# Kernel optimization log

Measured on AMD Instinct MI355X. Metric: run time of the kernel, lower is better.

Reference implementation:

```python
import jax, jax.numpy as jnp
import numpy as np

N_NODES = 100000
N_EDGES = 3200000
N_FEAT = 128
N_CLASS = 40
K_HOPS = 2


def setup_inputs() -> dict:
    key = jax.random.key(0)
    k1, k2, k3 = jax.random.split(key, 3)
    feature = jax.random.normal(k1, (N_NODES, N_FEAT), dtype=jnp.float32)
    # Glorot-ish linear params (SGConv.lin)
    weight = jax.random.normal(k2, (N_CLASS, N_FEAT), dtype=jnp.float32) * (1.0 / np.sqrt(N_FEAT))
    bias = jnp.zeros((N_CLASS,), dtype=jnp.float32)
    edge_index = jax.random.randint(k3, (2, N_EDGES), 0, N_NODES, dtype=jnp.int64)
    return {"feature": feature, "weight": weight, "bias": bias,
            "edge_index": edge_index, "use_feature": 1}


def reference(feature, weight, bias, edge_index, use_feature):
    # use_feature is a Python int flag; SGC uses feature when true (identity otherwise)
    x = feature if use_feature else jnp.eye(feature.shape[0], feature.shape[1], dtype=feature.dtype)
    N = x.shape[0]

    # gcn_norm: add self-loops, symmetric normalization D^-1/2 (A+I) D^-1/2
    loops = jnp.arange(N, dtype=edge_index.dtype)
    row = jnp.concatenate([edge_index[0], loops])  # source nodes
    col = jnp.concatenate([edge_index[1], loops])  # target nodes
    ew = jnp.ones(row.shape[0], dtype=x.dtype)
    deg = jax.ops.segment_sum(ew, col, num_segments=N)  # in-degree incl. self-loop
    deg_inv_sqrt = jnp.where(deg > 0, jax.lax.rsqrt(jnp.maximum(deg, 1e-12)), 0.0)
    norm = deg_inv_sqrt[row] * deg_inv_sqrt[col]  # [E+N]

    # K-hop propagation: out[col] += norm * x[row]
    for _ in range(K_HOPS):
        x = jax.ops.segment_sum(norm[:, None] * x[row], col, num_segments=N)

    logits = x @ weight.T + bias  # [N, C]
    return jax.nn.log_softmax(logits, axis=1)
```

## Files before the change

kernel.cpp:

```cpp
#include <hip/hip_runtime.h>
#include <hip/hip_bf16.h>
#include <hip/hip_fp16.h>
#include <math.h>


#define N_NODES 100000
#define N_FEAT  128
#define N_CLASS 40

#define RANGE   256
#define NBALLOC 512
#define NBUSED  391
#define RANGE_C 2048
#define NCALLOC 64
#define NCUSED  49
#define CAP     8704
#define CCAP    67072
#define P3AGRID 1024

typedef __attribute__((ext_vector_type(8))) short short8;
typedef __attribute__((ext_vector_type(4))) float floatx4;

__global__ void detect_zero_kernel(const int* __restrict__ ei, int* __restrict__ flag,
                                   int* __restrict__ bucketCount,
                                   int* __restrict__ coarseCnt) {
    int t = threadIdx.x;
    if (t < NBALLOC) bucketCount[t] = 0;
    if (t < NCALLOC) coarseCnt[t] = 0;
    if (t < 64) {
        int nz = (ei[2 * t + 1] != 0) ? 1 : 0;
        unsigned long long b = __ballot(nz);
        if (t == 0) *flag = (b == 0ull) ? 1 : 0;
    }
}

__device__ __forceinline__ int edge_word(const int* ei, int elem, int is64) {
    return is64 ? ei[2 * elem] : ei[elem];
}

__global__ __launch_bounds__(256) void p3a_scatter(
    const int* __restrict__ ei, int E, const int* __restrict__ flag,
    int* __restrict__ bucketCount, int* __restrict__ coarseCnt,
    unsigned int* __restrict__ tmpc)
{
    __shared__ int hf[NBALLOC];
    __shared__ int hc[NCALLOC];
    __shared__ int basec[NCALLOC];
    __shared__ int curc[NCALLOC];
    int t = threadIdx.x;
    for (int i = t; i < NBALLOC; i += 256) hf[i] = 0;
    if (t < NCALLOC) hc[t] = 0;
    __syncthreads();
    int is64 = *flag;
    int per = (E + gridDim.x - 1) / gridDim.x;
    int e0 = blockIdx.x * per;
    int e1 = min(E, e0 + per);
    for (int e = e0 + t; e < e1; e += 256) {
        int c = edge_word(ei, E + e, is64);
        atomicAdd(&hf[c >> 8], 1);
        atomicAdd(&hc[c >> 11], 1);
    }
    __syncthreads();
    if (t < NCALLOC) {
        basec[t] = hc[t] ? atomicAdd(&coarseCnt[t], hc[t]) : 0;
        curc[t] = 0;
    }
    for (int i = t; i < NBALLOC; i += 256)
        if (hf[i]) atomicAdd(&bucketCount[i], hf[i]);
    __syncthreads();
    for (int e = e0 + t; e < e1; e += 256) {
        int c = edge_word(ei, E + e, is64);
        int r = edge_word(ei, e, is64);
        int cb = c >> 11;
        int p = basec[cb] + atomicAdd(&curc[cb], 1);
        if (p < CCAP)
            tmpc[(size_t)cb * CCAP + p] = ((unsigned)(c & 2047) << 17) | (unsigned)r;
    }
}

__global__ __launch_bounds__(NBALLOC) void p2_scan(
    const int* __restrict__ bucketCount, int* __restrict__ bucketStart,
    int* __restrict__ bucketCursor, int* __restrict__ starts, int E)
{
    __shared__ int s[NBALLOC];
    int t = threadIdx.x;
    int v = bucketCount[t];
    s[t] = v;
    __syncthreads();
    for (int o = 1; o < NBALLOC; o <<= 1) {
        int y = (t >= o) ? s[t - o] : 0;
        __syncthreads();
        s[t] += y;
        __syncthreads();
    }
    int incl = s[t], excl = incl - v;
    bucketStart[t] = excl;
    bucketCursor[t] = excl;
    if (t == NBALLOC - 1) { bucketStart[NBALLOC] = incl; starts[N_NODES] = E; }
}

__global__ __launch_bounds__(256) void p3b_scatter(
    const unsigned int* __restrict__ tmpc, const int* __restrict__ coarseCnt,
    int* __restrict__ bucketCursor, unsigned int* __restrict__ tmp)
{
    __shared__ int fh[8];
    __shared__ int fb[8];
    __shared__ int fc[8];
    int cb = blockIdx.x >> 3;
    int j = blockIdx.x & 7;
    int t = threadIdx.x;
    int cnt = coarseCnt[cb];
    if (cnt > CCAP) cnt = CCAP;
    int chunk = (cnt + 7) >> 3;
    int r0 = j * chunk;
    int r1 = min(cnt, r0 + chunk);
    if (t < 8) fh[t] = 0;
    __syncthreads();
    const unsigned int* rec = tmpc + (size_t)cb * CCAP;
    for (int i = r0 + t; i < r1; i += 256) {
        int dlc = (int)(rec[i] >> 17);
        atomicAdd(&fh[dlc >> 8], 1);
    }
    __syncthreads();
    if (t < 8) {
        fb[t] = fh[t] ? atomicAdd(&bucketCursor[cb * 8 + t], fh[t]) : 0;
        fc[t] = 0;
    }
    __syncthreads();
    for (int i = r0 + t; i < r1; i += 256) {
        unsigned v = rec[i];
        int dlc = (int)(v >> 17);
        unsigned src = v & 0x1FFFFu;
        int fi = dlc >> 8;
        int dlf = dlc & 255;
        int p = fb[fi] + atomicAdd(&fc[fi], 1);
        tmp[p] = ((unsigned)dlf << 24) | src;
    }
}

__global__ __launch_bounds__(256) void p4_sort(
    const unsigned int* __restrict__ tmp, const int* __restrict__ bucketStart,
    int* __restrict__ starts, float* __restrict__ dis, int* __restrict__ srcsB, int N)
{
    __shared__ int srt[CAP];
    __shared__ int hist[256];
    __shared__ int sc[256];
    __shared__ int cur[256];
    int b = blockIdx.x, t = threadIdx.x;
    int g0 = b * RANGE;
    int gcnt = N - g0;
    if (gcnt > RANGE) gcnt = RANGE;
    int base = bucketStart[b];
    int n = bucketStart[b + 1] - base;
    hist[t] = 0;
    __syncthreads();
    for (int i = t; i < n; i += 256)
        atomicAdd(&hist[tmp[base + i] >> 24], 1);
    __syncthreads();
    int hv = hist[t];
    sc[t] = hv;
    __syncthreads();
    for (int o = 1; o < 256; o <<= 1) {
        int y = (t >= o) ? sc[t - o] : 0;
        __syncthreads();
        sc[t] += y;
        __syncthreads();
    }
    int excl = sc[t] - hv;
    if (t < gcnt) {
        starts[g0 + t] = base + excl;
        dis[g0 + t] = rsqrtf((float)(hv + 1));
    }
    cur[t] = excl;
    __syncthreads();
    if (n <= CAP) {
        for (int i = t; i < n; i += 256) {
            unsigned v = tmp[base + i];
            int p = atomicAdd(&cur[v >> 24], 1);
            srt[p] = (int)(v & 0xFFFFFFu) * 80;
        }
        __syncthreads();
        for (int i = t; i < n; i += 256) srcsB[base + i] = srt[i];
    } else {
        for (int i = t; i < n; i += 256) {
            unsigned v = tmp[base + i];
            int p = atomicAdd(&cur[v >> 24], 1);
            srcsB[base + p] = (int)(v & 0xFFFFFFu) * 80;
        }
    }
}

__device__ __forceinline__ unsigned short f2bf(float f) {
    unsigned u = __float_as_uint(f);
    unsigned r = u + 0x7FFFu + ((u >> 16) & 1u);
    return (unsigned short)(r >> 16);
}
__device__ __forceinline__ __half2 u2h(unsigned w) {
    union { unsigned u; __half2 h; } c; c.u = w; return c.h;
}
__device__ __forceinline__ unsigned h2u(__half2 h) {
    union { unsigned u; __half2 h; } c; c.h = h; return c.u;
}

__global__ __launch_bounds__(256) void transform_mfma(
    const float* __restrict__ x, const float* __restrict__ W,
    const float* __restrict__ dis, unsigned short* __restrict__ t0, int N)
{
    __shared__ uint4 Wl[3 * 4 * 64];
    int t = threadIdx.x;
    for (int i = t; i < 3 * 4 * 64; i += 256) {
        int lane = i & 63;
        int kc = (i >> 6) & 3;
        int nt = i >> 8;
        int n = nt * 16 + (lane & 15);
        int k = kc * 32 + (lane >> 4) * 8;
        union { unsigned short s[8]; uint4 v; } u;
        #pragma unroll
        for (int j = 0; j < 8; ++j)
            u.s[j] = (n < N_CLASS) ? f2bf(W[n * N_FEAT + k + j]) : (unsigned short)0;
        Wl[i] = u.v;
    }
    __syncthreads();
    int wave = (blockIdx.x * blockDim.x + threadIdx.x) >> 6;
    int lane = threadIdx.x & 63;
    int ntile = (N + 15) / 16;
    if (wave >= ntile) return;
    int m = lane & 15, quad = lane >> 4;
    int row = wave * 16 + m;
    const short8* Wf = reinterpret_cast<const short8*>(Wl);
    floatx4 acc0 = {0.f, 0.f, 0.f, 0.f}, acc1 = acc0, acc2 = acc0;
    #pragma unroll
    for (int kc = 0; kc < 4; ++kc) {
        const float4* xr = reinterpret_cast<const float4*>(
            x + (size_t)row * N_FEAT + kc * 32 + quad * 8);
        float4 a0 = xr[0], a1 = xr[1];
        short8 af;
        af[0] = f2bf(a0.x); af[1] = f2bf(a0.y); af[2] = f2bf(a0.z); af[3] = f2bf(a0.w);
        af[4] = f2bf(a1.x); af[5] = f2bf(a1.y); af[6] = f2bf(a1.z); af[7] = f2bf(a1.w);
        short8 b0 = Wf[(0 * 4 + kc) * 64 + lane];
        short8 b1 = Wf[(1 * 4 + kc) * 64 + lane];
        short8 b2 = Wf[(2 * 4 + kc) * 64 + lane];
        acc0 = __builtin_amdgcn_mfma_f32_16x16x32_bf16(af, b0, acc0, 0, 0, 0);
        acc1 = __builtin_amdgcn_mfma_f32_16x16x32_bf16(af, b1, acc1, 0, 0, 0);
        acc2 = __builtin_amdgcn_mfma_f32_16x16x32_bf16(af, b2, acc2, 0, 0, 0);
    }
    #pragma unroll
    for (int r = 0; r < 4; ++r) {
        int rw = wave * 16 + quad * 4 + r;
        float ds = dis[rw];
        unsigned short* tr = t0 + (size_t)rw * N_CLASS;
        tr[m] = __half_as_ushort(__float2half(ds * acc0[r]));
        tr[16 + m] = __half_as_ushort(__float2half(ds * acc1[r]));
        if (m < 8) tr[32 + m] = __half_as_ushort(__float2half(ds * acc2[r]));
    }
}

__device__ __forceinline__ __half2 foldh(__half2 a, int lane) {
    a = __hadd2(a, u2h((unsigned)__shfl((int)h2u(a), lane + 30)));
    a = __hadd2(a, u2h((unsigned)__shfl((int)h2u(a), lane + 15)));
    __half2 u = u2h((unsigned)__shfl((int)h2u(a), lane + 5));
    __half2 v = u2h((unsigned)__shfl((int)h2u(a), lane + 10));
    return __hadd2(__hadd2(a, u), v);
}

#define GATHER12H(tin)                                                         \
    int d = wave;                                                              \
    int g = lane / 5;                           \
    int sl = lane - g * 5;                                           \
    int slo = sl << 4;                             \
    int e0 = starts[d], e1 = starts[d + 1];                                    \
    const char* tb = (const char*)(tin);                                       \
    __half2 z2 = u2h(0u);                                                      \
    __half2 A0 = z2, A1 = z2, A2 = z2, A3 = z2;                                \
    __half2 B0 = z2, B1 = z2, B2 = z2, B3 = z2;                                \
    if (lane < 5) {                                       \
        uint4 r = *reinterpret_cast<const uint4*>(tb + d * 80 + slo);          \
        A0 = u2h(r.x); A1 = u2h(r.y); A2 = u2h(r.z); A3 = u2h(r.w);            \
    }                                                                          \
    int gg = (g < 12) ? g : 0;                      \
    int e = e0;                                                                \
    for (; e + 24 <= e1; e += 24) {         \
        int o1 = srcsB[e + gg];                                                \
        int o2 = srcsB[e + 12 + gg];                                           \
        uint4 r1 = *reinterpret_cast<const uint4*>(tb + (size_t)(unsigned)o1 + slo); \
        uint4 r2 = *reinterpret_cast<const uint4*>(tb + (size_t)(unsigned)o2 + slo); \
        A0 = __hadd2(A0, u2h(r1.x)); A1 = __hadd2(A1, u2h(r1.y));              \
        A2 = __hadd2(A2, u2h(r1.z)); A3 = __hadd2(A3, u2h(r1.w));              \
        B0 = __hadd2(B0, u2h(r2.x)); B1 = __hadd2(B1, u2h(r2.y));              \
        B2 = __hadd2(B2, u2h(r2.z)); B3 = __hadd2(B3, u2h(r2.w));              \
    }                                                                          \
    for (; e < e1; e += 12) {                      \
        int ee = e + gg;                                                       \
        int o1 = srcsB[min(ee, e1 - 1)];                                       \
        uint4 r1 = *reinterpret_cast<const uint4*>(tb + (size_t)(unsigned)o1 + slo); \
        if (!(ee < e1 && g < 12)) { r1.x = 0u; r1.y = 0u; r1.z = 0u; r1.w = 0u; } \
        A0 = __hadd2(A0, u2h(r1.x)); A1 = __hadd2(A1, u2h(r1.y));              \
        A2 = __hadd2(A2, u2h(r1.z)); A3 = __hadd2(A3, u2h(r1.w));              \
    }                                                                          \
    A0 = __hadd2(A0, B0); A1 = __hadd2(A1, B1);                                \
    A2 = __hadd2(A2, B2); A3 = __hadd2(A3, B3);                                \
    A0 = foldh(A0, lane); A1 = foldh(A1, lane);                                \
    A2 = foldh(A2, lane); A3 = foldh(A3, lane);

__global__ __launch_bounds__(256) void prop_hop_kernel(
    const unsigned short* __restrict__ tin, unsigned short* __restrict__ tout,
    const int* __restrict__ starts, const int* __restrict__ srcsB,
    const float* __restrict__ dis, int N)
{
    int wave = (blockIdx.x * blockDim.x + threadIdx.x) >> 6;
    int lane = threadIdx.x & 63;
    if (wave >= N) return;
    GATHER12H(tin)
    if (lane < 5) {
        float dd = dis[d];
        float sc = dd * dd;
        float2 f0 = __half22float2(A0), f1 = __half22float2(A1);
        float2 f2 = __half22float2(A2), f3 = __half22float2(A3);
        uint4 o;
        o.x = h2u(__floats2half2_rn(sc * f0.x, sc * f0.y));
        o.y = h2u(__floats2half2_rn(sc * f1.x, sc * f1.y));
        o.z = h2u(__floats2half2_rn(sc * f2.x, sc * f2.y));
        o.w = h2u(__floats2half2_rn(sc * f3.x, sc * f3.y));
        *reinterpret_cast<uint4*>((char*)tout + d * 80 + slo) = o;
    }
}

__global__ __launch_bounds__(256) void prop_final_kernel(
    const unsigned short* __restrict__ tin, float* __restrict__ out,
    const int* __restrict__ starts, const int* __restrict__ srcsB,
    const float* __restrict__ dis, const float* __restrict__ bias, int N)
{
    int wave = (blockIdx.x * blockDim.x + threadIdx.x) >> 6;
    int lane = threadIdx.x & 63;
    if (wave >= N) return;
    GATHER12H(tin)
    float dd = dis[d];
    float2 f0 = __half22float2(A0), f1 = __half22float2(A1);
    float2 f2 = __half22float2(A2), f3 = __half22float2(A3);
    float4 blo = reinterpret_cast<const float4*>(bias)[sl * 2];
    float4 bhi = reinterpret_cast<const float4*>(bias)[sl * 2 + 1];
    float v0 = dd * f0.x + blo.x, v1 = dd * f0.y + blo.y;
    float v2 = dd * f1.x + blo.z, v3 = dd * f1.y + blo.w;
    float v4 = dd * f2.x + bhi.x, v5 = dd * f2.y + bhi.y;
    float v6 = dd * f3.x + bhi.z, v7 = dd * f3.y + bhi.w;
    float mx = fmaxf(fmaxf(fmaxf(v0, v1), fmaxf(v2, v3)),
                     fmaxf(fmaxf(v4, v5), fmaxf(v6, v7)));
    if (lane >= 5) mx = -INFINITY;
    #pragma unroll
    for (int o = 4; o; o >>= 1) mx = fmaxf(mx, __shfl_xor(mx, o, 8));
    float sum = 0.f;
    if (lane < 5) {
        sum = expf(v0 - mx) + expf(v1 - mx) + expf(v2 - mx) + expf(v3 - mx)
            + expf(v4 - mx) + expf(v5 - mx) + expf(v6 - mx) + expf(v7 - mx);
    }
    #pragma unroll
    for (int o = 4; o; o >>= 1) sum += __shfl_xor(sum, o, 8);
    if (lane < 5) {
        float ls = mx + logf(sum);
        float* ro = out + (size_t)d * N_CLASS + sl * 8;
        *reinterpret_cast<float4*>(ro)     = make_float4(v0 - ls, v1 - ls, v2 - ls, v3 - ls);
        *reinterpret_cast<float4*>(ro + 4) = make_float4(v4 - ls, v5 - ls, v6 - ls, v7 - ls);
    }
}

extern "C" void kernel_launch(void* const* d_in, const int* in_sizes, int n_in,
                              void* d_out, int out_size, void* d_ws, size_t ws_size,
                              hipStream_t stream) {
    const float* feature = (const float*)d_in[0];
    const float* weight  = (const float*)d_in[1];
    const float* bias    = (const float*)d_in[2];
    const int*   ei      = (const int*)d_in[3];
    const int N = N_NODES;
    const int E = in_sizes[3] / 2;

    size_t off = 0;
    auto take = [&](size_t bytes) { size_t o = off; off += (bytes + 255) & ~(size_t)255; return o; };
    char* ws = (char*)d_ws;
    int*   flag      = (int*)  (ws + take(4));
    int*   bCount    = (int*)  (ws + take((size_t)NBALLOC * 4));
    int*   bStart    = (int*)  (ws + take((size_t)(NBALLOC + 1) * 4));
    int*   bCursor   = (int*)  (ws + take((size_t)NBALLOC * 4));
    int*   coarseCnt = (int*)  (ws + take((size_t)NCALLOC * 4));
    int*   starts    = (int*)  (ws + take((size_t)(N + 1) * 4));
    float* dis       = (float*)(ws + take((size_t)N * 4));
    size_t srcsBytes = (size_t)E * 4;
    size_t tmpcBytes = (size_t)NCALLOC * CCAP * 4;
    size_t bigBytes = srcsBytes > tmpcBytes ? srcsBytes : tmpcBytes;
    char* bigBase = ws + take(bigBytes);
    int* srcsB = (int*)bigBase;
    unsigned int* tmpc = (unsigned int*)bigBase;
    unsigned short* t0 = (unsigned short*)(ws + take((size_t)N * N_CLASS * 2));
    unsigned short* t1 = (unsigned short*)(ws + take((size_t)N * N_CLASS * 2));
    unsigned int* tmp = (unsigned int*)t0;

    detect_zero_kernel<<<1, 512, 0, stream>>>(ei, flag, bCount, coarseCnt);
    p3a_scatter<<<P3AGRID, 256, 0, stream>>>(ei, E, flag, bCount, coarseCnt, tmpc);
    p2_scan<<<1, NBALLOC, 0, stream>>>(bCount, bStart, bCursor, starts, E);
    p3b_scatter<<<NCUSED * 8, 256, 0, stream>>>(tmpc, coarseCnt, bCursor, tmp);
    p4_sort<<<NBUSED, 256, 0, stream>>>(tmp, bStart, starts, dis, srcsB, N);

    const int ntile = (N + 15) / 16;
    const int tblocks = (ntile * 64 + 255) / 256;
    transform_mfma<<<tblocks, 256, 0, stream>>>(feature, weight, dis, t0, N);
    const int nodeBlocks = (N * 64 + 255) / 256;
    prop_hop_kernel<<<nodeBlocks, 256, 0, stream>>>(t0, t1, starts, srcsB, dis, N);
    prop_final_kernel<<<nodeBlocks, 256, 0, stream>>>(t1, (float*)d_out,
                                                      starts, srcsB, dis, bias, N);
}
```

Baseline: 329.8 us.

## Map 12 nodes per wave with 5 lanes each, accumulate in fp32

The gather kernels change from one node per wave (12 edge-groups of 5 lanes, then a cross-group shuffle reduction) to 12 nodes per wave, where each 5-lane group walks its own node's edge list sequentially. Edge indices are loaded four at a time with aligned vector loads, and accumulation moves from half2 to fp32. The log-softmax reduction becomes a 5-lane rotation shuffle. This removes the cross-lane fold and most idle lanes, but adds load imbalance between nodes in a wave and longer serial latency chains per lane.

```diff
diff --git a/kernel.cpp b/kernel.cpp
--- a/kernel.cpp
+++ b/kernel.cpp
@@ -255,73 +255,74 @@
     }
 }
 
-__device__ __forceinline__ __half2 foldh(__half2 a, int lane) {
-    a = __hadd2(a, u2h((unsigned)__shfl((int)h2u(a), lane + 30)));
-    a = __hadd2(a, u2h((unsigned)__shfl((int)h2u(a), lane + 15)));
-    __half2 u = u2h((unsigned)__shfl((int)h2u(a), lane + 5));
-    __half2 v = u2h((unsigned)__shfl((int)h2u(a), lane + 10));
-    return __hadd2(__hadd2(a, u), v);
-}
-
-#define GATHER12H(tin)                                                         \
-    int d = wave;                                                              \
-    int g = lane / 5;                           \
-    int sl = lane - g * 5;                                           \
-    int slo = sl << 4;                             \
-    int e0 = starts[d], e1 = starts[d + 1];                                    \
-    const char* tb = (const char*)(tin);                                       \
-    __half2 z2 = u2h(0u);                                                      \
-    __half2 A0 = z2, A1 = z2, A2 = z2, A3 = z2;                                \
-    __half2 B0 = z2, B1 = z2, B2 = z2, B3 = z2;                                \
-    if (lane < 5) {                                       \
-        uint4 r = *reinterpret_cast<const uint4*>(tb + d * 80 + slo);          \
-        A0 = u2h(r.x); A1 = u2h(r.y); A2 = u2h(r.z); A3 = u2h(r.w);            \
+struct F8 { float v0, v1, v2, v3, v4, v5, v6, v7; };
+
+__device__ __forceinline__ void acc8(F8& a, uint4 r) {
+    float2 f0 = __half22float2(u2h(r.x));
+    float2 f1 = __half22float2(u2h(r.y));
+    float2 f2 = __half22float2(u2h(r.z));
+    float2 f3 = __half22float2(u2h(r.w));
+    a.v0 += f0.x; a.v1 += f0.y; a.v2 += f1.x; a.v3 += f1.y;
+    a.v4 += f2.x; a.v5 += f2.y; a.v6 += f3.x; a.v7 += f3.y;
+}
+
+#define GATHER5(tin)                                                           \
+    int wv = (blockIdx.x * blockDim.x + threadIdx.x) >> 6;                     \
+    int lane = threadIdx.x & 63;                                               \
+    int g = lane / 5;                                                          \
+    int sl = lane - g * 5;                                                     \
+    if (g > 11) { g = 11; sl = 0; }                                            \
+    int d = wv * 12 + g;                                                       \
+    int act = (lane < 60) && (d < N);                                          \
+    int dc = min(d, N - 1);                                                    \
+    int e0 = starts[dc];                                                       \
+    int e1 = starts[dc + 1];                                                   \
+    if (d >= N) e1 = e0;                                                       \
+    int slo = sl << 4;                                                         \
+    const char* tbs = (const char*)(tin) + slo;                                \
+    F8 A = {0,0,0,0,0,0,0,0}, B = {0,0,0,0,0,0,0,0};                           \
+    {                                                                          \
+        uint4 rs = *reinterpret_cast<const uint4*>(tbs + (size_t)dc * 80);     \
+        acc8(A, rs);                                      \
     }                                                                          \
-    int gg = (g < 12) ? g : 0;                      \
     int e = e0;                                                                \
-    for (; e + 24 <= e1; e += 24) {         \
-        int o1 = srcsB[e + gg];                                                \
-        int o2 = srcsB[e + 12 + gg];                                           \
-        uint4 r1 = *reinterpret_cast<const uint4*>(tb + (size_t)(unsigned)o1 + slo); \
-        uint4 r2 = *reinterpret_cast<const uint4*>(tb + (size_t)(unsigned)o2 + slo); \
-        A0 = __hadd2(A0, u2h(r1.x)); A1 = __hadd2(A1, u2h(r1.y));              \
-        A2 = __hadd2(A2, u2h(r1.z)); A3 = __hadd2(A3, u2h(r1.w));              \
-        B0 = __hadd2(B0, u2h(r2.x)); B1 = __hadd2(B1, u2h(r2.y));              \
-        B2 = __hadd2(B2, u2h(r2.z)); B3 = __hadd2(B3, u2h(r2.w));              \
+    int ea = min(e1, (e0 + 3) & ~3);                                           \
+    for (; e < ea; ++e) {                                   \
+        int o = srcsB[e];                                                      \
+        uint4 r = *reinterpret_cast<const uint4*>(tbs + (unsigned)o);          \
+        acc8(A, r);                                                            \
     }                                                                          \
-    for (; e < e1; e += 12) {                      \
-        int ee = e + gg;                                                       \
-        int o1 = srcsB[min(ee, e1 - 1)];                                       \
-        uint4 r1 = *reinterpret_cast<const uint4*>(tb + (size_t)(unsigned)o1 + slo); \
-        if (!(ee < e1 && g < 12)) { r1.x = 0u; r1.y = 0u; r1.z = 0u; r1.w = 0u; } \
-        A0 = __hadd2(A0, u2h(r1.x)); A1 = __hadd2(A1, u2h(r1.y));              \
-        A2 = __hadd2(A2, u2h(r1.z)); A3 = __hadd2(A3, u2h(r1.w));              \
+    for (; e + 4 <= e1; e += 4) {                     \
+        int4 o4 = *reinterpret_cast<const int4*>(srcsB + e);                   \
+        uint4 r0 = *reinterpret_cast<const uint4*>(tbs + (unsigned)o4.x);      \
+        uint4 r1 = *reinterpret_cast<const uint4*>(tbs + (unsigned)o4.y);      \
+        uint4 r2 = *reinterpret_cast<const uint4*>(tbs + (unsigned)o4.z);      \
+        uint4 r3 = *reinterpret_cast<const uint4*>(tbs + (unsigned)o4.w);      \
+        acc8(A, r0); acc8(B, r1); acc8(A, r2); acc8(B, r3);                    \
     }                                                                          \
-    A0 = __hadd2(A0, B0); A1 = __hadd2(A1, B1);                                \
-    A2 = __hadd2(A2, B2); A3 = __hadd2(A3, B3);                                \
-    A0 = foldh(A0, lane); A1 = foldh(A1, lane);                                \
-    A2 = foldh(A2, lane); A3 = foldh(A3, lane);
+    for (; e < e1; ++e) {                                 \
+        int o = srcsB[e];                                                      \
+        uint4 r = *reinterpret_cast<const uint4*>(tbs + (unsigned)o);          \
+        acc8(A, r);                                                            \
+    }                                                                          \
+    A.v0 += B.v0; A.v1 += B.v1; A.v2 += B.v2; A.v3 += B.v3;                    \
+    A.v4 += B.v4; A.v5 += B.v5; A.v6 += B.v6; A.v7 += B.v7;
 
 __global__ __launch_bounds__(256) void prop_hop_kernel(
     const unsigned short* __restrict__ tin, unsigned short* __restrict__ tout,
     const int* __restrict__ starts, const int* __restrict__ srcsB,
     const float* __restrict__ dis, int N)
 {
-    int wave = (blockIdx.x * blockDim.x + threadIdx.x) >> 6;
-    int lane = threadIdx.x & 63;
-    if (wave >= N) return;
-    GATHER12H(tin)
-    if (lane < 5) {
-        float dd = dis[d];
+    GATHER5(tin)
+    if (act) {
+        float dd = dis[dc];
         float sc = dd * dd;
-        float2 f0 = __half22float2(A0), f1 = __half22float2(A1);
-        float2 f2 = __half22float2(A2), f3 = __half22float2(A3);
         uint4 o;
-        o.x = h2u(__floats2half2_rn(sc * f0.x, sc * f0.y));
-        o.y = h2u(__floats2half2_rn(sc * f1.x, sc * f1.y));
-        o.z = h2u(__floats2half2_rn(sc * f2.x, sc * f2.y));
-        o.w = h2u(__floats2half2_rn(sc * f3.x, sc * f3.y));
-        *reinterpret_cast<uint4*>((char*)tout + d * 80 + slo) = o;
+        o.x = h2u(__floats2half2_rn(sc * A.v0, sc * A.v1));
+        o.y = h2u(__floats2half2_rn(sc * A.v2, sc * A.v3));
+        o.z = h2u(__floats2half2_rn(sc * A.v4, sc * A.v5));
+        o.w = h2u(__floats2half2_rn(sc * A.v6, sc * A.v7));
+        *reinterpret_cast<uint4*>((char*)tout + (size_t)d * 80 + slo) = o;
     }
 }
 
@@ -330,33 +331,27 @@
     const int* __restrict__ starts, const int* __restrict__ srcsB,
     const float* __restrict__ dis, const float* __restrict__ bias, int N)
 {
-    int wave = (blockIdx.x * blockDim.x + threadIdx.x) >> 6;
-    int lane = threadIdx.x & 63;
-    if (wave >= N) return;
-    GATHER12H(tin)
-    float dd = dis[d];
-    float2 f0 = __half22float2(A0), f1 = __half22float2(A1);
-    float2 f2 = __half22float2(A2), f3 = __half22float2(A3);
+    GATHER5(tin)
+    float dd = dis[dc];
     float4 blo = reinterpret_cast<const float4*>(bias)[sl * 2];
     float4 bhi = reinterpret_cast<const float4*>(bias)[sl * 2 + 1];
-    float v0 = dd * f0.x + blo.x, v1 = dd * f0.y + blo.y;
-    float v2 = dd * f1.x + blo.z, v3 = dd * f1.y + blo.w;
-    float v4 = dd * f2.x + bhi.x, v5 = dd * f2.y + bhi.y;
-    float v6 = dd * f3.x + bhi.z, v7 = dd * f3.y + bhi.w;
+    float v0 = dd * A.v0 + blo.x, v1 = dd * A.v1 + blo.y;
+    float v2 = dd * A.v2 + blo.z, v3 = dd * A.v3 + blo.w;
+    float v4 = dd * A.v4 + bhi.x, v5 = dd * A.v5 + bhi.y;
+    float v6 = dd * A.v6 + bhi.z, v7 = dd * A.v7 + bhi.w;
     float mx = fmaxf(fmaxf(fmaxf(v0, v1), fmaxf(v2, v3)),
                      fmaxf(fmaxf(v4, v5), fmaxf(v6, v7)));
-    if (lane >= 5) mx = -INFINITY;
+    int rot = g * 5 + ((sl + 1 == 5) ? 0 : sl + 1);
+    float tmx = mx;
     #pragma unroll
-    for (int o = 4; o; o >>= 1) mx = fmaxf(mx, __shfl_xor(mx, o, 8));
-    float sum = 0.f;
-    if (lane < 5) {
-        sum = expf(v0 - mx) + expf(v1 - mx) + expf(v2 - mx) + expf(v3 - mx)
+    for (int k = 0; k < 4; ++k) { tmx = __shfl(tmx, rot); mx = fmaxf(mx, tmx); }
+    float s = expf(v0 - mx) + expf(v1 - mx) + expf(v2 - mx) + expf(v3 - mx)
             + expf(v4 - mx) + expf(v5 - mx) + expf(v6 - mx) + expf(v7 - mx);
-    }
+    float ts = s;
     #pragma unroll
-    for (int o = 4; o; o >>= 1) sum += __shfl_xor(sum, o, 8);
-    if (lane < 5) {
-        float ls = mx + logf(sum);
+    for (int k = 0; k < 4; ++k) { ts = __shfl(ts, rot); s += ts; }
+    if (act) {
+        float ls = mx + logf(s);
         float* ro = out + (size_t)d * N_CLASS + sl * 8;
         *reinterpret_cast<float4*>(ro)     = make_float4(v0 - ls, v1 - ls, v2 - ls, v3 - ls);
         *reinterpret_cast<float4*>(ro + 4) = make_float4(v4 - ls, v5 - ls, v6 - ls, v7 - ls);
@@ -402,7 +397,8 @@
     const int ntile = (N + 15) / 16;
     const int tblocks = (ntile * 64 + 255) / 256;
     transform_mfma<<<tblocks, 256, 0, stream>>>(feature, weight, dis, t0, N);
-    const int nodeBlocks = (N * 64 + 255) / 256;
+    const int nwaves = (N + 11) / 12;
+    const int nodeBlocks = (nwaves * 64 + 255) / 256;
     prop_hop_kernel<<<nodeBlocks, 256, 0, stream>>>(t0, t1, starts, srcsB, dis, N);
     prop_final_kernel<<<nodeBlocks, 256, 0, stream>>>(t1, (float*)d_out,
                                                       starts, srcsB, dis, bias, N);
```

New measurement: 354.1 us. +7.4%, slower.

## Split each propagation hop into two passes by source-node half for cache locality

Applied to the files above, without the earlier changes.

The sort now partitions each destination's edge list into sources below and above the node midpoint and records a mid offset per node. Each hop runs as two kernels: the first gathers only from low-half sources and stores a partial sum, and the second gathers from high-half sources and adds the partial. The intent is to shrink the gather working set of the feature table in each pass so it stays resident in cache. In exchange it adds extra kernel launches and an extra write and read of the partial results, including an fp32 partial round trip through the output buffer in the final hop.

```diff
diff --git a/kernel.cpp b/kernel.cpp
--- a/kernel.cpp
+++ b/kernel.cpp
@@ -17,6 +17,7 @@
 #define CAP     8704
 #define CCAP    67072
 #define P3AGRID 1024
+#define HALF_SPLIT 50000
 
 typedef __attribute__((ext_vector_type(8))) short short8;
 typedef __attribute__((ext_vector_type(4))) float floatx4;
@@ -140,12 +141,13 @@
 
 __global__ __launch_bounds__(256) void p4_sort(
     const unsigned int* __restrict__ tmp, const int* __restrict__ bucketStart,
-    int* __restrict__ starts, float* __restrict__ dis, int* __restrict__ srcsB, int N)
+    int* __restrict__ starts, int* __restrict__ mid, float* __restrict__ dis,
+    int* __restrict__ srcsB, int N)
 {
     __shared__ int srt[CAP];
-    __shared__ int hist[256];
+    __shared__ int hist[512];
     __shared__ int sc[256];
-    __shared__ int cur[256];
+    __shared__ int cur[512];
     int b = blockIdx.x, t = threadIdx.x;
     int g0 = b * RANGE;
     int gcnt = N - g0;
@@ -153,12 +155,16 @@
     int base = bucketStart[b];
     int n = bucketStart[b + 1] - base;
     hist[t] = 0;
-    __syncthreads();
-    for (int i = t; i < n; i += 256)
-        atomicAdd(&hist[tmp[base + i] >> 24], 1);
-    __syncthreads();
-    int hv = hist[t];
-    sc[t] = hv;
+    hist[t + 256] = 0;
+    __syncthreads();
+    for (int i = t; i < n; i += 256) {
+        unsigned v = tmp[base + i];
+        int key = (int)((v >> 24) << 1) | (((v & 0xFFFFFFu) >= HALF_SPLIT) ? 1 : 0);
+        atomicAdd(&hist[key], 1);
+    }
+    __syncthreads();
+    int c0 = hist[2 * t], c1 = hist[2 * t + 1];
+    sc[t] = c0 + c1;
     __syncthreads();
     for (int o = 1; o < 256; o <<= 1) {
         int y = (t >= o) ? sc[t - o] : 0;
@@ -166,26 +172,32 @@
         sc[t] += y;
         __syncthreads();
     }
-    int excl = sc[t] - hv;
+    int excl = sc[t] - (c0 + c1);
     if (t < gcnt) {
         starts[g0 + t] = base + excl;
-        dis[g0 + t] = rsqrtf((float)(hv + 1));
-    }
-    cur[t] = excl;
+        mid[g0 + t] = base + excl + c0;
+        dis[g0 + t] = rsqrtf((float)(c0 + c1 + 1));
+    }
+    cur[2 * t] = excl;
+    cur[2 * t + 1] = excl + c0;
     __syncthreads();
     if (n <= CAP) {
         for (int i = t; i < n; i += 256) {
             unsigned v = tmp[base + i];
-            int p = atomicAdd(&cur[v >> 24], 1);
-            srt[p] = (int)(v & 0xFFFFFFu) * 80;
+            int src = (int)(v & 0xFFFFFFu);
+            int key = (int)((v >> 24) << 1) | ((src >= HALF_SPLIT) ? 1 : 0);
+            int p = atomicAdd(&cur[key], 1);
+            srt[p] = src * 80;
         }
         __syncthreads();
         for (int i = t; i < n; i += 256) srcsB[base + i] = srt[i];
     } else {
         for (int i = t; i < n; i += 256) {
             unsigned v = tmp[base + i];
-            int p = atomicAdd(&cur[v >> 24], 1);
-            srcsB[base + p] = (int)(v & 0xFFFFFFu) * 80;
+            int src = (int)(v & 0xFFFFFFu);
+            int key = (int)((v >> 24) << 1) | ((src >= HALF_SPLIT) ? 1 : 0);
+            int p = atomicAdd(&cur[key], 1);
+            srcsB[base + p] = src * 80;
         }
     }
 }
@@ -263,17 +275,20 @@
     return __hadd2(__hadd2(a, u), v);
 }
 
-#define GATHER12H(tin)                                                         \
+#define GATHER12H(tin, eBp, eEp, SELF)                                         \
+    int wave = (blockIdx.x * blockDim.x + threadIdx.x) >> 6;                   \
+    int lane = threadIdx.x & 63;                                               \
+    if (wave >= N) return;                                                     \
     int d = wave;                                                              \
     int g = lane / 5;                           \
     int sl = lane - g * 5;                                           \
     int slo = sl << 4;                             \
-    int e0 = starts[d], e1 = starts[d + 1];                                    \
+    int e0 = (eBp)[d], e1 = (eEp)[d];                                          \
     const char* tb = (const char*)(tin);                                       \
     __half2 z2 = u2h(0u);                                                      \
     __half2 A0 = z2, A1 = z2, A2 = z2, A3 = z2;                                \
     __half2 B0 = z2, B1 = z2, B2 = z2, B3 = z2;                                \
-    if (lane < 5) {                                       \
+    if (SELF && lane < 5) {                               \
         uint4 r = *reinterpret_cast<const uint4*>(tb + d * 80 + slo);          \
         A0 = u2h(r.x); A1 = u2h(r.y); A2 = u2h(r.z); A3 = u2h(r.w);            \
     }                                                                          \
@@ -302,16 +317,29 @@
     A0 = foldh(A0, lane); A1 = foldh(A1, lane);                                \
     A2 = foldh(A2, lane); A3 = foldh(A3, lane);
 
-__global__ __launch_bounds__(256) void prop_hop_kernel(
+__global__ __launch_bounds__(256) void prop_hop0(
     const unsigned short* __restrict__ tin, unsigned short* __restrict__ tout,
-    const int* __restrict__ starts, const int* __restrict__ srcsB,
-    const float* __restrict__ dis, int N)
-{
-    int wave = (blockIdx.x * blockDim.x + threadIdx.x) >> 6;
-    int lane = threadIdx.x & 63;
-    if (wave >= N) return;
-    GATHER12H(tin)
+    const int* __restrict__ starts, const int* __restrict__ mid,
+    const int* __restrict__ srcsB, int N)
+{
+    GATHER12H(tin, starts, mid, 1)
     if (lane < 5) {
+        uint4 o;
+        o.x = h2u(A0); o.y = h2u(A1); o.z = h2u(A2); o.w = h2u(A3);
+        *reinterpret_cast<uint4*>((char*)tout + d * 80 + slo) = o;
+    }
+}
+
+__global__ __launch_bounds__(256) void prop_hop1(
+    const unsigned short* __restrict__ tin, unsigned short* __restrict__ tout,
+    const int* __restrict__ starts, const int* __restrict__ mid,
+    const int* __restrict__ srcsB, const float* __restrict__ dis, int N)
+{
+    GATHER12H(tin, mid, starts + 1, 0)
+    if (lane < 5) {
+        uint4 pr = *reinterpret_cast<const uint4*>((const char*)tout + d * 80 + slo);
+        A0 = __hadd2(A0, u2h(pr.x)); A1 = __hadd2(A1, u2h(pr.y));
+        A2 = __hadd2(A2, u2h(pr.z)); A3 = __hadd2(A3, u2h(pr.w));
         float dd = dis[d];
         float sc = dd * dd;
         float2 f0 = __half22float2(A0), f1 = __half22float2(A1);
@@ -325,38 +353,54 @@
     }
 }
 
-__global__ __launch_bounds__(256) void prop_final_kernel(
+__global__ __launch_bounds__(256) void prop_fin0(
     const unsigned short* __restrict__ tin, float* __restrict__ out,
-    const int* __restrict__ starts, const int* __restrict__ srcsB,
-    const float* __restrict__ dis, const float* __restrict__ bias, int N)
-{
-    int wave = (blockIdx.x * blockDim.x + threadIdx.x) >> 6;
-    int lane = threadIdx.x & 63;
-    if (wave >= N) return;
-    GATHER12H(tin)
+    const int* __restrict__ starts, const int* __restrict__ mid,
+    const int* __restrict__ srcsB, int N)
+{
+    GATHER12H(tin, starts, mid, 1)
+    if (lane < 5) {
+        float2 f0 = __half22float2(A0), f1 = __half22float2(A1);
+        float2 f2 = __half22float2(A2), f3 = __half22float2(A3);
+        float* ro = out + (size_t)d * N_CLASS + sl * 8;
+        *reinterpret_cast<float4*>(ro)     = make_float4(f0.x, f0.y, f1.x, f1.y);
+        *reinterpret_cast<float4*>(ro + 4) = make_float4(f2.x, f2.y, f3.x, f3.y);
+    }
+}
+
+__global__ __launch_bounds__(256) void prop_fin1(
+    const unsigned short* __restrict__ tin, float* __restrict__ out,
+    const int* __restrict__ starts, const int* __restrict__ mid,
+    const int* __restrict__ srcsB, const float* __restrict__ dis,
+    const float* __restrict__ bias, int N)
+{
+    GATHER12H(tin, mid, starts + 1, 0)
     float dd = dis[d];
+    const float* pp = out + (size_t)d * N_CLASS + sl * 8;
+    float4 plo = *reinterpret_cast<const float4*>(pp);
+    float4 phi = *reinterpret_cast<const float4*>(pp + 4);
+    float4 blo = reinterpret_cast<const float4*>(bias)[sl * 2];
+    float4 bhi = reinterpret_cast<const float4*>(bias)[sl * 2 + 1];
     float2 f0 = __half22float2(A0), f1 = __half22float2(A1);
     float2 f2 = __half22float2(A2), f3 = __half22float2(A3);
-    float4 blo = reinterpret_cast<const float4*>(bias)[sl * 2];
-    float4 bhi = reinterpret_cast<const float4*>(bias)[sl * 2 + 1];
-    float v0 = dd * f0.x + blo.x, v1 = dd * f0.y + blo.y;
-    float v2 = dd * f1.x + blo.z, v3 = dd * f1.y + blo.w;
-    float v4 = dd * f2.x + bhi.x, v5 = dd * f2.y + bhi.y;
-    float v6 = dd * f3.x + bhi.z, v7 = dd * f3.y + bhi.w;
+    float v0 = dd * (plo.x + f0.x) + blo.x, v1 = dd * (plo.y + f0.y) + blo.y;
+    float v2 = dd * (plo.z + f1.x) + blo.z, v3 = dd * (plo.w + f1.y) + blo.w;
+    float v4 = dd * (phi.x + f2.x) + bhi.x, v5 = dd * (phi.y + f2.y) + bhi.y;
+    float v6 = dd * (phi.z + f3.x) + bhi.z, v7 = dd * (phi.w + f3.y) + bhi.w;
     float mx = fmaxf(fmaxf(fmaxf(v0, v1), fmaxf(v2, v3)),
                      fmaxf(fmaxf(v4, v5), fmaxf(v6, v7)));
     if (lane >= 5) mx = -INFINITY;
     #pragma unroll
     for (int o = 4; o; o >>= 1) mx = fmaxf(mx, __shfl_xor(mx, o, 8));
-    float sum = 0.f;
+    float s = 0.f;
     if (lane < 5) {
-        sum = expf(v0 - mx) + expf(v1 - mx) + expf(v2 - mx) + expf(v3 - mx)
-            + expf(v4 - mx) + expf(v5 - mx) + expf(v6 - mx) + expf(v7 - mx);
+        s = expf(v0 - mx) + expf(v1 - mx) + expf(v2 - mx) + expf(v3 - mx)
+          + expf(v4 - mx) + expf(v5 - mx) + expf(v6 - mx) + expf(v7 - mx);
     }
     #pragma unroll
-    for (int o = 4; o; o >>= 1) sum += __shfl_xor(sum, o, 8);
+    for (int o = 4; o; o >>= 1) s += __shfl_xor(s, o, 8);
     if (lane < 5) {
-        float ls = mx + logf(sum);
+        float ls = mx + logf(s);
         float* ro = out + (size_t)d * N_CLASS + sl * 8;
         *reinterpret_cast<float4*>(ro)     = make_float4(v0 - ls, v1 - ls, v2 - ls, v3 - ls);
         *reinterpret_cast<float4*>(ro + 4) = make_float4(v4 - ls, v5 - ls, v6 - ls, v7 - ls);
@@ -382,6 +426,7 @@
     int*   bCursor   = (int*)  (ws + take((size_t)NBALLOC * 4));
     int*   coarseCnt = (int*)  (ws + take((size_t)NCALLOC * 4));
     int*   starts    = (int*)  (ws + take((size_t)(N + 1) * 4));
+    int*   mid       = (int*)  (ws + take((size_t)N * 4));
     float* dis       = (float*)(ws + take((size_t)N * 4));
     size_t srcsBytes = (size_t)E * 4;
     size_t tmpcBytes = (size_t)NCALLOC * CCAP * 4;
@@ -397,13 +442,15 @@
     p3a_scatter<<<P3AGRID, 256, 0, stream>>>(ei, E, flag, bCount, coarseCnt, tmpc);
     p2_scan<<<1, NBALLOC, 0, stream>>>(bCount, bStart, bCursor, starts, E);
     p3b_scatter<<<NCUSED * 8, 256, 0, stream>>>(tmpc, coarseCnt, bCursor, tmp);
-    p4_sort<<<NBUSED, 256, 0, stream>>>(tmp, bStart, starts, dis, srcsB, N);
+    p4_sort<<<NBUSED, 256, 0, stream>>>(tmp, bStart, starts, mid, dis, srcsB, N);
 
     const int ntile = (N + 15) / 16;
     const int tblocks = (ntile * 64 + 255) / 256;
     transform_mfma<<<tblocks, 256, 0, stream>>>(feature, weight, dis, t0, N);
     const int nodeBlocks = (N * 64 + 255) / 256;
-    prop_hop_kernel<<<nodeBlocks, 256, 0, stream>>>(t0, t1, starts, srcsB, dis, N);
-    prop_final_kernel<<<nodeBlocks, 256, 0, stream>>>(t1, (float*)d_out,
-                                                      starts, srcsB, dis, bias, N);
-}
+    prop_hop0<<<nodeBlocks, 256, 0, stream>>>(t0, t1, starts, mid, srcsB, N);
+    prop_hop1<<<nodeBlocks, 256, 0, stream>>>(t0, t1, starts, mid, srcsB, dis, N);
+    prop_fin0<<<nodeBlocks, 256, 0, stream>>>(t1, (float*)d_out, starts, mid, srcsB, N);
+    prop_fin1<<<nodeBlocks, 256, 0, stream>>>(t1, (float*)d_out, starts, mid, srcsB,
+                                              dis, bias, N);
+}
```

New measurement: 373.6 us. 1.13x slower.
